# Kernel tuning notes

Hardware: AMD Instinct MI355X
Metric: run time of the kernel (lower is better)

The kernel has to match this reference:

```python
import jax, jax.numpy as jnp
import numpy as np


def setup_inputs() -> dict:
    key = jax.random.key(0)
    k1, k2, k3 = jax.random.split(key, 3)
    B, L, S, H, E, D = 2, 512, 512, 8, 32, 64
    queries = jax.random.normal(k1, (B, L, H, E), dtype=jnp.float32)
    keys = jax.random.normal(k2, (B, S, H, E), dtype=jnp.float32)
    values = jax.random.normal(k3, (B, S, H, D), dtype=jnp.float32)
    v = jnp.ones((E,), dtype=jnp.float32)
    attn_mask_add = jnp.zeros((L, S), dtype=jnp.float32)
    key_lengths_add = jnp.zeros((B, S), dtype=jnp.float32)
    return {
        "queries": queries,
        "keys": keys,
        "values": values,
        "v": v,
        "attn_mask_add": attn_mask_add,
        "key_lengths_add": key_lengths_add,
    }


def reference(queries, keys, values, v, attn_mask_add, key_lengths_add):
    # Additive (Bahdanau) attention.
    # queries: (B,L,H,E), keys: (B,S,H,E), values: (B,S,H,D)
    # Broadcast add -> tanh -> contract with v: (B,L,S,H,E) -> (B,H,L,S)
    feat = jnp.tanh(queries[:, :, None, :, :] + keys[:, None, :, :, :])  # (B,L,S,H,E)
    scores = jnp.einsum("blshe,e->bhls", feat, v)  # (B,H,L,S)
    scores = scores + attn_mask_add[None, None, :, :]          # (L,S) attn mask
    scores = scores + key_lengths_add[:, None, None, :]        # (B,S) key-length mask
    A = jax.nn.softmax(scores, axis=-1)  # (B,H,L,S); dropout is identity (p=0 / eval)
    V = jnp.einsum("bhls,bshd->blhd", A, values)  # (B,L,H,D)
    return V
```

## Files before the change

kernel.cpp:

```cpp
#include <hip/hip_runtime.h>


#define BB 2
#define LL 512
#define SS 512
#define HH 8
#define EE 32
#define DD 64

#define WS_EK_OFF 0
#define WS_EQ_OFF (2u * 1024u * 1024u)
#define WS_VT_OFF (4u * 1024u * 1024u)

typedef __attribute__((ext_vector_type(8))) short bf16x8;
typedef __attribute__((ext_vector_type(4))) float f32x4;
typedef __attribute__((ext_vector_type(4))) unsigned u32x4;

__device__ __forceinline__ unsigned short f2bf(float f) {
    unsigned u = __float_as_uint(f);
    u += 0x7FFFu + ((u >> 16) & 1u);
    return (unsigned short)(u >> 16);
}
__device__ __forceinline__ float fast_exp2(float x) {
#if __has_builtin(__builtin_amdgcn_exp2f)
    return __builtin_amdgcn_exp2f(x);
#else
    return exp2f(x);
#endif
}
__device__ __forceinline__ float fast_rcp(float x) {
    return __builtin_amdgcn_rcpf(x);
}
__device__ __forceinline__ float bcastf(float x) {
    return __int_as_float(__builtin_amdgcn_readfirstlane(__float_as_int(x)));
}

#define SCV 2.885390081777927f

__global__ __launch_bounds__(256) void prep_kernel(
    const float* __restrict__ q, const float* __restrict__ k,
    const float* __restrict__ vals, float* __restrict__ ws)
{
    unsigned gid = blockIdx.x * 256 + threadIdx.x;
    if (gid < 32768u) {
        unsigned i  = gid;
        unsigned s  = i & 511u;
        unsigned e8 = (i >> 9) & 3u;
        unsigned h  = (i >> 11) & 7u;
        unsigned b  = i >> 14;
        const float* kr = k + (((size_t)b * SS + s) * HH + h) * EE + e8 * 8;
        float4 k0 = *(const float4*)kr;
        float4 k1 = *(const float4*)(kr + 4);
        u32x4 pk;
        pk[0] = (unsigned)f2bf(fast_exp2(SCV * k0.x)) |
                ((unsigned)f2bf(fast_exp2(SCV * k0.y)) << 16);
        pk[1] = (unsigned)f2bf(fast_exp2(SCV * k0.z)) |
                ((unsigned)f2bf(fast_exp2(SCV * k0.w)) << 16);
        pk[2] = (unsigned)f2bf(fast_exp2(SCV * k1.x)) |
                ((unsigned)f2bf(fast_exp2(SCV * k1.y)) << 16);
        pk[3] = (unsigned)f2bf(fast_exp2(SCV * k1.z)) |
                ((unsigned)f2bf(fast_exp2(SCV * k1.w)) << 16);
        ((u32x4*)((char*)ws + WS_EK_OFF))[i] = pk;
    } else if (gid < 98304u) {
        unsigned i = gid - 32768u;
        float4 qv = ((const float4*)q)[i];
        float4 ev = make_float4(fast_exp2(SCV * qv.x), fast_exp2(SCV * qv.y),
                                fast_exp2(SCV * qv.z), fast_exp2(SCV * qv.w));
        ((float4*)(ws + WS_EQ_OFF / 4))[i] = ev;
    } else {
        unsigned i      = gid - 98304u;
        unsigned lane   = i & 63u;
        unsigned c      = (i >> 6) & 15u;
        unsigned dchunk = (i >> 10) & 3u;
        unsigned h      = (i >> 12) & 7u;
        unsigned b      = i >> 15;
        unsigned qd = lane >> 4, n = lane & 15;
        unsigned d  = dchunk * 16 + n;
        unsigned s0 = c * 32 + qd * 8;
        const float* vb = vals + (((size_t)b * SS + s0) * HH + h) * DD + d;
        u32x4 pk;
        #pragma unroll
        for (int j2 = 0; j2 < 4; j2++) {
            float f0 = vb[(size_t)(2 * j2) * (HH * DD)];
            float f1 = vb[(size_t)(2 * j2 + 1) * (HH * DD)];
            pk[j2] = (unsigned)f2bf(f0) | ((unsigned)f2bf(f1) << 16);
        }
        ((u32x4*)((char*)ws + WS_VT_OFF))[i] = pk;
    }
}

__global__ __launch_bounds__(256) void addattn_kernel(
    const u32x4* __restrict__ ws_ekb,
    const float* __restrict__ ws_eqf,
    const bf16x8* __restrict__ ws_vtf,
    const float* __restrict__ vvec,
    const float* __restrict__ mask,
    const float* __restrict__ klen,
    float* __restrict__ out)
{
    __shared__ u32x4 sek[4 * SS];
    __shared__ unsigned short sAb[8][SS];

    const int tid  = threadIdx.x;
    const int w    = tid >> 6;
    const int lane = tid & 63;
    const int bh   = blockIdx.x >> 6;
    const int lblk = blockIdx.x & 63;
    const int b    = bh >> 3;
    const int h    = bh & 7;
    const int l0   = lblk * 8;
    const int lw   = l0 + 2 * w;

    {
        const u32x4* esrc = ws_ekb + (size_t)(b * HH + h) * (4 * SS);
        #pragma unroll
        for (int t = 0; t < 8; t++)
            sek[tid + t * 256] = esrc[tid + t * 256];
    }

    float eq0[EE], eq1[EE], v2s[EE];
    {
        const float* q0 = ws_eqf + (((size_t)b * LL + lw) * HH + h) * EE;
        const float* q1 = q0 + HH * EE;
        #pragma unroll
        for (int e = 0; e < EE; e += 4) {
            float4 t0 = *(const float4*)(q0 + e);
            float4 t1 = *(const float4*)(q1 + e);
            eq0[e] = bcastf(t0.x); eq0[e+1] = bcastf(t0.y);
            eq0[e+2] = bcastf(t0.z); eq0[e+3] = bcastf(t0.w);
            eq1[e] = bcastf(t1.x); eq1[e+1] = bcastf(t1.y);
            eq1[e+2] = bcastf(t1.z); eq1[e+3] = bcastf(t1.w);
        }
        const float4* vr = (const float4*)vvec;
        #pragma unroll
        for (int e4 = 0; e4 < EE / 4; e4++) {
            float4 t = vr[e4];
            v2s[e4*4]   = -2.f * t.x; v2s[e4*4+1] = -2.f * t.y;
            v2s[e4*4+2] = -2.f * t.z; v2s[e4*4+3] = -2.f * t.w;
        }
    }
    __syncthreads();

    float sc[2][SS / 64];
    for (int i = 0; i < SS / 64; i++) {
        const int s = lane + i * 64;
        u32x4 g0 = sek[s];
        u32x4 g1 = sek[SS + s];
        u32x4 g2 = sek[2 * SS + s];
        u32x4 g3 = sek[3 * SS + s];
        float a0[4] = {0.f, 0.f, 0.f, 0.f};
        float a1[4] = {0.f, 0.f, 0.f, 0.f};
        #define ELEM(E, F)                                                    \
        {                                                                     \
            float p0 = __builtin_fmaf(eq0[E], F, 1.f);                        \
            float p1 = __builtin_fmaf(eq1[E], F, 1.f);                        \
            a0[(E) & 3] = __builtin_fmaf(v2s[E], fast_rcp(p0), a0[(E) & 3]);  \
            a1[(E) & 3] = __builtin_fmaf(v2s[E], fast_rcp(p1), a1[(E) & 3]);  \
        }
        #define PAIR(u, E)                                                    \
        {                                                                     \
            float flo = __uint_as_float((u) << 16);                           \
            float fhi = __uint_as_float((u) & 0xffff0000u);                   \
            ELEM(E, flo) ELEM((E) + 1, fhi)                                   \
        }
        #define GRP(g, base)                                                  \
        {                                                                     \
            PAIR(g[0], (base) + 0) PAIR(g[1], (base) + 2)                     \
            PAIR(g[2], (base) + 4) PAIR(g[3], (base) + 6)                     \
        }
        GRP(g0, 0) GRP(g1, 8) GRP(g2, 16) GRP(g3, 24)
        #undef GRP
        #undef PAIR
        #undef ELEM
        sc[0][i] = (a0[0] + a0[1]) + (a0[2] + a0[3]);
        sc[1][i] = (a1[0] + a1[1]) + (a1[2] + a1[3]);
    }

    {
        const float* kl = klen + (size_t)b * SS;
        float klv[SS / 64];
        #pragma unroll
        for (int i = 0; i < SS / 64; i++) klv[i] = kl[lane + i * 64];

        #pragma unroll
        for (int r = 0; r < 2; r++) {
            const float* mrow = mask + (size_t)(lw + r) * SS;
            float mx = -1e30f;
            #pragma unroll
            for (int i = 0; i < SS / 64; i++) {
                sc[r][i] += mrow[lane + i * 64] + klv[i];
                mx = fmaxf(mx, sc[r][i]);
            }
            #pragma unroll
            for (int off = 1; off < 64; off <<= 1) mx = fmaxf(mx, __shfl_xor(mx, off, 64));
            float ssum = 0.f;
            #pragma unroll
            for (int i = 0; i < SS / 64; i++) {
                sc[r][i] = __expf(sc[r][i] - mx);
                ssum += sc[r][i];
            }
            #pragma unroll
            for (int off = 1; off < 64; off <<= 1) ssum += __shfl_xor(ssum, off, 64);
            float inv = fast_rcp(ssum);
            const int row = 2 * w + r;
            const int fsw = (row * 5) & 7;
            #pragma unroll
            for (int i = 0; i < SS / 64; i++) {
                int col = lane + i * 64;
                int pos = (((col >> 3) ^ fsw) << 3) | (col & 7);
                sAb[row][pos] = f2bf(sc[r][i] * inv);
            }
        }
    }
    __syncthreads();

    const int am  = lane & 15;
    const int qd  = lane >> 4;
    const int dof = w * 16 + am;
    const int fam = (am * 5) & 7;
    const bf16x8* vf =
        ws_vtf + ((size_t)((b * HH + h) * 4 + w) * 16) * 64 + lane;
    f32x4 acc = {0.f, 0.f, 0.f, 0.f};
    bf16x8 bcur = vf[0];
    for (int c = 0; c < SS / 32; c++) {
        bf16x8 bnxt = bcur;
        if (c < SS / 32 - 1) bnxt = vf[(c + 1) * 64];
        bf16x8 af = {0, 0, 0, 0, 0, 0, 0, 0};
        if (am < 8)
            af = *(const bf16x8*)&sAb[am][((c * 4 + qd) ^ fam) << 3];
        acc = __builtin_amdgcn_mfma_f32_16x16x32_bf16(af, bcur, acc, 0, 0, 0);
        bcur = bnxt;
    }
    if (qd < 2) {
        float* orow = out + (((size_t)b * LL + l0 + qd * 4) * HH + h) * DD + dof;
        #pragma unroll
        for (int r = 0; r < 4; r++)
            orow[(size_t)r * (HH * DD)] = acc[r];
    }
}

extern "C" void kernel_launch(void* const* d_in, const int* in_sizes, int n_in,
                              void* d_out, int out_size, void* d_ws, size_t ws_size,
                              hipStream_t stream) {
    const float* q    = (const float*)d_in[0];
    const float* k    = (const float*)d_in[1];
    const float* vals = (const float*)d_in[2];
    const float* vvec = (const float*)d_in[3];
    const float* mask = (const float*)d_in[4];
    const float* klen = (const float*)d_in[5];
    float* outp = (float*)d_out;

    float* ws = (float*)d_ws;
    prep_kernel<<<dim3(640), dim3(256), 0, stream>>>(q, k, vals, ws);

    const u32x4* ws_ekb = (const u32x4*)((char*)d_ws + WS_EK_OFF);
    const float* ws_eqf = (const float*)((char*)d_ws + WS_EQ_OFF);
    const bf16x8* ws_vtf = (const bf16x8*)((char*)d_ws + WS_VT_OFF);
    addattn_kernel<<<dim3(BB * HH * (LL / 8)), dim3(256), 0, stream>>>(
        ws_ekb, ws_eqf, ws_vtf, vvec, mask, klen, outp);
}
```

Baseline: 93.75 us.

## Halve rows per block, stage keys in halves, pair-merge reciprocals

Each wave now handles one query row instead of two, and the grid doubles to 2048 blocks. Keys are staged into shared memory in two halves of S, and that same buffer is reused for the bf16 probability matrix, cutting LDS from about 40KB to 16KB. Per-element tanh terms are merged in pairs so one reciprocal covers two elements (a/x + b/y = (a*y+b*x)/(x*y)), halving rcp count. The aim is more occupancy and fewer transcendental ops, at the cost of loading keys twice as often per query row, running half-empty MFMA tiles, and a possible overflow risk in the product of two denominators.

```diff
diff --git a/kernel.cpp b/kernel.cpp
--- a/kernel.cpp
+++ b/kernel.cpp
@@ -98,118 +98,108 @@
     const float* __restrict__ klen,
     float* __restrict__ out)
 {
-    __shared__ u32x4 sek[4 * SS];
-    __shared__ unsigned short sAb[8][SS];
+    __shared__ u32x4 sek[4][256];
+    unsigned short* sAb = (unsigned short*)sek;
 
     const int tid  = threadIdx.x;
     const int w    = tid >> 6;
     const int lane = tid & 63;
-    const int bh   = blockIdx.x >> 6;
-    const int lblk = blockIdx.x & 63;
+    const int bh   = blockIdx.x >> 7;
+    const int lblk = blockIdx.x & 127;
     const int b    = bh >> 3;
     const int h    = bh & 7;
-    const int l0   = lblk * 8;
-    const int lw   = l0 + 2 * w;
-
-    {
-        const u32x4* esrc = ws_ekb + (size_t)(b * HH + h) * (4 * SS);
-        #pragma unroll
-        for (int t = 0; t < 8; t++)
-            sek[tid + t * 256] = esrc[tid + t * 256];
-    }
-
-    float eq0[EE], eq1[EE], v2s[EE];
-    {
-        const float* q0 = ws_eqf + (((size_t)b * LL + lw) * HH + h) * EE;
-        const float* q1 = q0 + HH * EE;
-        #pragma unroll
-        for (int e = 0; e < EE; e += 4) {
-            float4 t0 = *(const float4*)(q0 + e);
-            float4 t1 = *(const float4*)(q1 + e);
-            eq0[e] = bcastf(t0.x); eq0[e+1] = bcastf(t0.y);
-            eq0[e+2] = bcastf(t0.z); eq0[e+3] = bcastf(t0.w);
-            eq1[e] = bcastf(t1.x); eq1[e+1] = bcastf(t1.y);
-            eq1[e+2] = bcastf(t1.z); eq1[e+3] = bcastf(t1.w);
-        }
-        const float4* vr = (const float4*)vvec;
-        #pragma unroll
-        for (int e4 = 0; e4 < EE / 4; e4++) {
-            float4 t = vr[e4];
-            v2s[e4*4]   = -2.f * t.x; v2s[e4*4+1] = -2.f * t.y;
-            v2s[e4*4+2] = -2.f * t.z; v2s[e4*4+3] = -2.f * t.w;
-        }
-    }
-    __syncthreads();
-
-    float sc[2][SS / 64];
-    for (int i = 0; i < SS / 64; i++) {
-        const int s = lane + i * 64;
-        u32x4 g0 = sek[s];
-        u32x4 g1 = sek[SS + s];
-        u32x4 g2 = sek[2 * SS + s];
-        u32x4 g3 = sek[3 * SS + s];
-        float a0[4] = {0.f, 0.f, 0.f, 0.f};
-        float a1[4] = {0.f, 0.f, 0.f, 0.f};
-        #define ELEM(E, F)                                                    \
-        {                                                                     \
-            float p0 = __builtin_fmaf(eq0[E], F, 1.f);                        \
-            float p1 = __builtin_fmaf(eq1[E], F, 1.f);                        \
-            a0[(E) & 3] = __builtin_fmaf(v2s[E], fast_rcp(p0), a0[(E) & 3]);  \
-            a1[(E) & 3] = __builtin_fmaf(v2s[E], fast_rcp(p1), a1[(E) & 3]);  \
-        }
-        #define PAIR(u, E)                                                    \
-        {                                                                     \
-            float flo = __uint_as_float((u) << 16);                           \
-            float fhi = __uint_as_float((u) & 0xffff0000u);                   \
-            ELEM(E, flo) ELEM((E) + 1, fhi)                                   \
-        }
-        #define GRP(g, base)                                                  \
-        {                                                                     \
-            PAIR(g[0], (base) + 0) PAIR(g[1], (base) + 2)                     \
-            PAIR(g[2], (base) + 4) PAIR(g[3], (base) + 6)                     \
-        }
-        GRP(g0, 0) GRP(g1, 8) GRP(g2, 16) GRP(g3, 24)
-        #undef GRP
-        #undef PAIR
-        #undef ELEM
-        sc[0][i] = (a0[0] + a0[1]) + (a0[2] + a0[3]);
-        sc[1][i] = (a1[0] + a1[1]) + (a1[2] + a1[3]);
-    }
-
-    {
-        const float* kl = klen + (size_t)b * SS;
-        float klv[SS / 64];
-        #pragma unroll
-        for (int i = 0; i < SS / 64; i++) klv[i] = kl[lane + i * 64];
-
-        #pragma unroll
-        for (int r = 0; r < 2; r++) {
-            const float* mrow = mask + (size_t)(lw + r) * SS;
-            float mx = -1e30f;
+    const int l0   = lblk * 4;
+    const int l    = l0 + w;
+
+    const u32x4* slab = ws_ekb + (size_t)(b * HH + h) * (4 * 512);
+    const float* eqbase = ws_eqf + (((size_t)b * LL + l) * HH + h) * EE;
+
+    float sc[SS / 64];
+    #pragma unroll
+    for (int i = 0; i < SS / 64; i++) sc[i] = 0.f;
+
+    for (int hs = 0; hs < 2; hs++) {
+        if (hs) __syncthreads();
+        #pragma unroll
+        for (int t = 0; t < 4; t++) {
+            int idx = tid + t * 256;
+            int e8  = idx >> 8;
+            int sl  = idx & 255;
+            sek[e8][sl] = slab[e8 * 512 + hs * 256 + sl];
+        }
+        __syncthreads();
+
+        for (int p = 0; p < 2; p++) {
+            float eqs[16], v2h[16];
             #pragma unroll
-            for (int i = 0; i < SS / 64; i++) {
-                sc[r][i] += mrow[lane + i * 64] + klv[i];
-                mx = fmaxf(mx, sc[r][i]);
+            for (int e = 0; e < 16; e += 4) {
+                float4 t0 = *(const float4*)(eqbase + p * 16 + e);
+                float4 tv = *(const float4*)(vvec + p * 16 + e);
+                eqs[e]   = bcastf(t0.x); eqs[e+1] = bcastf(t0.y);
+                eqs[e+2] = bcastf(t0.z); eqs[e+3] = bcastf(t0.w);
+                v2h[e]   = bcastf(-2.f * tv.x); v2h[e+1] = bcastf(-2.f * tv.y);
+                v2h[e+2] = bcastf(-2.f * tv.z); v2h[e+3] = bcastf(-2.f * tv.w);
             }
             #pragma unroll
-            for (int off = 1; off < 64; off <<= 1) mx = fmaxf(mx, __shfl_xor(mx, off, 64));
-            float ssum = 0.f;
-            #pragma unroll
-            for (int i = 0; i < SS / 64; i++) {
-                sc[r][i] = __expf(sc[r][i] - mx);
-                ssum += sc[r][i];
+            for (int i = 0; i < 4; i++) {
+                const int sl = lane + i * 64;
+                u32x4 gA = sek[2 * p][sl];
+                u32x4 gB = sek[2 * p + 1][sl];
+                float a0 = 0.f, a1 = 0.f;
+                #define PAIR(u, le, A)                                        \
+                {                                                             \
+                    float eklo = __uint_as_float((u) << 16);                  \
+                    float ekhi = __uint_as_float((u) & 0xffff0000u);          \
+                    float qa = __builtin_fmaf(eqs[le], eklo, 1.f);            \
+                    float qb = __builtin_fmaf(eqs[(le) + 1], ekhi, 1.f);      \
+                    float nm = __builtin_fmaf(v2h[le], qb, v2h[(le) + 1] * qa); \
+                    A = __builtin_fmaf(nm, fast_rcp(qa * qb), A);             \
+                }
+                PAIR(gA[0], 0, a0) PAIR(gA[1], 2, a1)
+                PAIR(gA[2], 4, a0) PAIR(gA[3], 6, a1)
+                PAIR(gB[0], 8, a0) PAIR(gB[1], 10, a1)
+                PAIR(gB[2], 12, a0) PAIR(gB[3], 14, a1)
+                #undef PAIR
+                sc[hs * 4 + i] += a0 + a1;
             }
-            #pragma unroll
-            for (int off = 1; off < 64; off <<= 1) ssum += __shfl_xor(ssum, off, 64);
-            float inv = fast_rcp(ssum);
-            const int row = 2 * w + r;
-            const int fsw = (row * 5) & 7;
-            #pragma unroll
-            for (int i = 0; i < SS / 64; i++) {
-                int col = lane + i * 64;
-                int pos = (((col >> 3) ^ fsw) << 3) | (col & 7);
-                sAb[row][pos] = f2bf(sc[r][i] * inv);
-            }
+        }
+    }
+
+    float prob[SS / 64];
+    {
+        const float* mrow = mask + (size_t)l * SS;
+        const float* kl   = klen + (size_t)b * SS;
+        float mx = -1e30f;
+        #pragma unroll
+        for (int i = 0; i < SS / 64; i++) {
+            int s = lane + i * 64;
+            sc[i] += mrow[s] + kl[s];
+            mx = fmaxf(mx, sc[i]);
+        }
+        #pragma unroll
+        for (int off = 1; off < 64; off <<= 1) mx = fmaxf(mx, __shfl_xor(mx, off, 64));
+        float ssum = 0.f;
+        #pragma unroll
+        for (int i = 0; i < SS / 64; i++) {
+            prob[i] = __expf(sc[i] - mx);
+            ssum += prob[i];
+        }
+        #pragma unroll
+        for (int off = 1; off < 64; off <<= 1) ssum += __shfl_xor(ssum, off, 64);
+        float inv = fast_rcp(ssum);
+        #pragma unroll
+        for (int i = 0; i < SS / 64; i++) prob[i] *= inv;
+    }
+
+    __syncthreads();
+
+    {
+        const int fsw = (w * 5) & 7;
+        #pragma unroll
+        for (int i = 0; i < SS / 64; i++) {
+            int col = lane + i * 64;
+            int pos = (((col >> 3) ^ fsw) << 3) | (col & 7);
+            sAb[w * SS + pos] = f2bf(prob[i]);
         }
     }
     __syncthreads();
@@ -226,13 +216,13 @@
         bf16x8 bnxt = bcur;
         if (c < SS / 32 - 1) bnxt = vf[(c + 1) * 64];
         bf16x8 af = {0, 0, 0, 0, 0, 0, 0, 0};
-        if (am < 8)
-            af = *(const bf16x8*)&sAb[am][((c * 4 + qd) ^ fam) << 3];
+        if (am < 4)
+            af = *(const bf16x8*)&sAb[am * SS + ((((c * 4 + qd) ^ fam)) << 3)];
         acc = __builtin_amdgcn_mfma_f32_16x16x32_bf16(af, bcur, acc, 0, 0, 0);
         bcur = bnxt;
     }
-    if (qd < 2) {
-        float* orow = out + (((size_t)b * LL + l0 + qd * 4) * HH + h) * DD + dof;
+    if (qd == 0) {
+        float* orow = out + (((size_t)b * LL + l0) * HH + h) * DD + dof;
         #pragma unroll
         for (int r = 0; r < 4; r++)
             orow[(size_t)r * (HH * DD)] = acc[r];
@@ -256,6 +246,6 @@
     const u32x4* ws_ekb = (const u32x4*)((char*)d_ws + WS_EK_OFF);
     const float* ws_eqf = (const float*)((char*)d_ws + WS_EQ_OFF);
     const bf16x8* ws_vtf = (const bf16x8*)((char*)d_ws + WS_VT_OFF);
-    addattn_kernel<<<dim3(BB * HH * (LL / 8)), dim3(256), 0, stream>>>(
+    addattn_kernel<<<dim3(BB * HH * (LL / 4)), dim3(256), 0, stream>>>(
         ws_ekb, ws_eqf, ws_vtf, vvec, mask, klen, outp);
 }
```

After: 97.81 us. 1.04x slower.

## Split attention into score and PV kernels, pair tanh reciprocals, drop max pass

Applied to the files above, without the earlier changes.

Splits the fused kernel in two. The score kernel writes unnormalized bf16 probabilities and row sums to the workspace, and a separate PV kernel runs full 16-row MFMA tiles and normalizes at output. The tanh rational terms are combined in pairs so one reciprocal serves two elements. The softmax max reduction is replaced by clamping at 80, which risks overflow or precision loss when scores are large or masks very negative. The split adds an extra launch and a global round trip for the probability matrix, in exchange for removing the wasted half-empty MFMA rows and half the reciprocals.

```diff
diff --git a/kernel.cpp b/kernel.cpp
--- a/kernel.cpp
+++ b/kernel.cpp
@@ -11,6 +11,8 @@
 #define WS_EK_OFF 0
 #define WS_EQ_OFF (2u * 1024u * 1024u)
 #define WS_VT_OFF (4u * 1024u * 1024u)
+#define WS_PR_OFF (8u * 1024u * 1024u)
+#define WS_SM_OFF (16u * 1024u * 1024u)
 
 typedef __attribute__((ext_vector_type(8))) short bf16x8;
 typedef __attribute__((ext_vector_type(4))) float f32x4;
@@ -89,17 +91,16 @@
     }
 }
 
-__global__ __launch_bounds__(256) void addattn_kernel(
+__global__ __launch_bounds__(256) void score_kernel(
     const u32x4* __restrict__ ws_ekb,
     const float* __restrict__ ws_eqf,
-    const bf16x8* __restrict__ ws_vtf,
     const float* __restrict__ vvec,
     const float* __restrict__ mask,
     const float* __restrict__ klen,
-    float* __restrict__ out)
+    unsigned short* __restrict__ ws_prob,
+    float* __restrict__ ws_sum)
 {
     __shared__ u32x4 sek[4 * SS];
-    __shared__ unsigned short sAb[8][SS];
 
     const int tid  = threadIdx.x;
     const int w    = tid >> 6;
@@ -108,11 +109,10 @@
     const int lblk = blockIdx.x & 63;
     const int b    = bh >> 3;
     const int h    = bh & 7;
-    const int l0   = lblk * 8;
-    const int lw   = l0 + 2 * w;
+    const int lw   = lblk * 8 + 2 * w;
 
     {
-        const u32x4* esrc = ws_ekb + (size_t)(b * HH + h) * (4 * SS);
+        const u32x4* esrc = ws_ekb + (size_t)bh * (4 * SS);
         #pragma unroll
         for (int t = 0; t < 8; t++)
             sek[tid + t * 256] = esrc[tid + t * 256];
@@ -135,45 +135,44 @@
         #pragma unroll
         for (int e4 = 0; e4 < EE / 4; e4++) {
             float4 t = vr[e4];
-            v2s[e4*4]   = -2.f * t.x; v2s[e4*4+1] = -2.f * t.y;
-            v2s[e4*4+2] = -2.f * t.z; v2s[e4*4+3] = -2.f * t.w;
+            v2s[e4*4]   = bcastf(-2.f * t.x); v2s[e4*4+1] = bcastf(-2.f * t.y);
+            v2s[e4*4+2] = bcastf(-2.f * t.z); v2s[e4*4+3] = bcastf(-2.f * t.w);
         }
     }
     __syncthreads();
 
-    float sc[2][SS / 64];
+    float sc0[SS / 64], sc1[SS / 64];
     for (int i = 0; i < SS / 64; i++) {
         const int s = lane + i * 64;
         u32x4 g0 = sek[s];
         u32x4 g1 = sek[SS + s];
         u32x4 g2 = sek[2 * SS + s];
         u32x4 g3 = sek[3 * SS + s];
-        float a0[4] = {0.f, 0.f, 0.f, 0.f};
-        float a1[4] = {0.f, 0.f, 0.f, 0.f};
-        #define ELEM(E, F)                                                    \
+        float a0A = 0.f, a0B = 0.f, a1A = 0.f, a1B = 0.f;
+        #define PAIR2(u, le, A0, A1)                                          \
         {                                                                     \
-            float p0 = __builtin_fmaf(eq0[E], F, 1.f);                        \
-            float p1 = __builtin_fmaf(eq1[E], F, 1.f);                        \
-            a0[(E) & 3] = __builtin_fmaf(v2s[E], fast_rcp(p0), a0[(E) & 3]);  \
-            a1[(E) & 3] = __builtin_fmaf(v2s[E], fast_rcp(p1), a1[(E) & 3]);  \
-        }
-        #define PAIR(u, E)                                                    \
-        {                                                                     \
-            float flo = __uint_as_float((u) << 16);                           \
-            float fhi = __uint_as_float((u) & 0xffff0000u);                   \
-            ELEM(E, flo) ELEM((E) + 1, fhi)                                   \
-        }
-        #define GRP(g, base)                                                  \
-        {                                                                     \
-            PAIR(g[0], (base) + 0) PAIR(g[1], (base) + 2)                     \
-            PAIR(g[2], (base) + 4) PAIR(g[3], (base) + 6)                     \
-        }
-        GRP(g0, 0) GRP(g1, 8) GRP(g2, 16) GRP(g3, 24)
-        #undef GRP
-        #undef PAIR
-        #undef ELEM
-        sc[0][i] = (a0[0] + a0[1]) + (a0[2] + a0[3]);
-        sc[1][i] = (a1[0] + a1[1]) + (a1[2] + a1[3]);
+            float eklo = __uint_as_float((u) << 16);                          \
+            float ekhi = __uint_as_float((u) & 0xffff0000u);                  \
+            float qa0 = __builtin_fmaf(eq0[le], eklo, 1.f);                   \
+            float qb0 = __builtin_fmaf(eq0[(le) + 1], ekhi, 1.f);             \
+            float nm0 = __builtin_fmaf(v2s[le], qb0, v2s[(le) + 1] * qa0);    \
+            A0 = __builtin_fmaf(nm0, fast_rcp(qa0 * qb0), A0);                \
+            float qa1 = __builtin_fmaf(eq1[le], eklo, 1.f);                   \
+            float qb1 = __builtin_fmaf(eq1[(le) + 1], ekhi, 1.f);             \
+            float nm1 = __builtin_fmaf(v2s[le], qb1, v2s[(le) + 1] * qa1);    \
+            A1 = __builtin_fmaf(nm1, fast_rcp(qa1 * qb1), A1);                \
+        }
+        PAIR2(g0[0], 0, a0A, a1A)  PAIR2(g0[1], 2, a0B, a1B)
+        PAIR2(g0[2], 4, a0A, a1A)  PAIR2(g0[3], 6, a0B, a1B)
+        PAIR2(g1[0], 8, a0A, a1A)  PAIR2(g1[1], 10, a0B, a1B)
+        PAIR2(g1[2], 12, a0A, a1A) PAIR2(g1[3], 14, a0B, a1B)
+        PAIR2(g2[0], 16, a0A, a1A) PAIR2(g2[1], 18, a0B, a1B)
+        PAIR2(g2[2], 20, a0A, a1A) PAIR2(g2[3], 22, a0B, a1B)
+        PAIR2(g3[0], 24, a0A, a1A) PAIR2(g3[1], 26, a0B, a1B)
+        PAIR2(g3[2], 28, a0A, a1A) PAIR2(g3[3], 30, a0B, a1B)
+        #undef PAIR2
+        sc0[i] = a0A + a0B;
+        sc1[i] = a1A + a1B;
     }
 
     {
@@ -184,59 +183,68 @@
 
         #pragma unroll
         for (int r = 0; r < 2; r++) {
+            float* sc = r ? sc1 : sc0;
             const float* mrow = mask + (size_t)(lw + r) * SS;
-            float mx = -1e30f;
-            #pragma unroll
-            for (int i = 0; i < SS / 64; i++) {
-                sc[r][i] += mrow[lane + i * 64] + klv[i];
-                mx = fmaxf(mx, sc[r][i]);
-            }
-            #pragma unroll
-            for (int off = 1; off < 64; off <<= 1) mx = fmaxf(mx, __shfl_xor(mx, off, 64));
             float ssum = 0.f;
             #pragma unroll
             for (int i = 0; i < SS / 64; i++) {
-                sc[r][i] = __expf(sc[r][i] - mx);
-                ssum += sc[r][i];
+                float v = fminf(sc[i] + mrow[lane + i * 64] + klv[i], 80.f);
+                sc[i] = __expf(v);
+                ssum += sc[i];
             }
             #pragma unroll
             for (int off = 1; off < 64; off <<= 1) ssum += __shfl_xor(ssum, off, 64);
-            float inv = fast_rcp(ssum);
-            const int row = 2 * w + r;
-            const int fsw = (row * 5) & 7;
+            unsigned short* pr = ws_prob + ((size_t)bh * LL + lw + r) * SS;
             #pragma unroll
-            for (int i = 0; i < SS / 64; i++) {
-                int col = lane + i * 64;
-                int pos = (((col >> 3) ^ fsw) << 3) | (col & 7);
-                sAb[row][pos] = f2bf(sc[r][i] * inv);
-            }
-        }
-    }
-    __syncthreads();
-
-    const int am  = lane & 15;
-    const int qd  = lane >> 4;
+            for (int i = 0; i < SS / 64; i++)
+                pr[lane + i * 64] = f2bf(sc[i]);
+            if (lane == 0) ws_sum[(size_t)bh * LL + lw + r] = ssum;
+        }
+    }
+}
+
+__global__ __launch_bounds__(256) void pv_kernel(
+    const unsigned short* __restrict__ ws_prob,
+    const float* __restrict__ ws_sum,
+    const bf16x8* __restrict__ ws_vtf,
+    float* __restrict__ out)
+{
+    const int tid  = threadIdx.x;
+    const int w    = tid >> 6;
+    const int lane = tid & 63;
+    const int bh   = blockIdx.x >> 5;
+    const int lt   = blockIdx.x & 31;
+    const int b    = bh >> 3;
+    const int h    = bh & 7;
+    const int l0   = lt * 16;
+
+    const int am = lane & 15;
+    const int qd = lane >> 4;
+    const unsigned short* ap = ws_prob + ((size_t)bh * LL + l0 + am) * SS + qd * 8;
+    const bf16x8* vf = ws_vtf + ((size_t)(bh * 4 + w) * 16) * 64 + lane;
+
+    f32x4 acc = {0.f, 0.f, 0.f, 0.f};
+    bf16x8 af[4], bv[4];
+    #pragma unroll
+    for (int c = 0; c < 4; c++) {
+        af[c] = *(const bf16x8*)(ap + c * 32);
+        bv[c] = vf[c * 64];
+    }
+    #pragma unroll
+    for (int c = 0; c < SS / 32; c++) {
+        acc = __builtin_amdgcn_mfma_f32_16x16x32_bf16(af[c & 3], bv[c & 3],
+                                                      acc, 0, 0, 0);
+        if (c + 4 < SS / 32) {
+            af[c & 3] = *(const bf16x8*)(ap + (c + 4) * 32);
+            bv[c & 3] = vf[(c + 4) * 64];
+        }
+    }
     const int dof = w * 16 + am;
-    const int fam = (am * 5) & 7;
-    const bf16x8* vf =
-        ws_vtf + ((size_t)((b * HH + h) * 4 + w) * 16) * 64 + lane;
-    f32x4 acc = {0.f, 0.f, 0.f, 0.f};
-    bf16x8 bcur = vf[0];
-    for (int c = 0; c < SS / 32; c++) {
-        bf16x8 bnxt = bcur;
-        if (c < SS / 32 - 1) bnxt = vf[(c + 1) * 64];
-        bf16x8 af = {0, 0, 0, 0, 0, 0, 0, 0};
-        if (am < 8)
-            af = *(const bf16x8*)&sAb[am][((c * 4 + qd) ^ fam) << 3];
-        acc = __builtin_amdgcn_mfma_f32_16x16x32_bf16(af, bcur, acc, 0, 0, 0);
-        bcur = bnxt;
-    }
-    if (qd < 2) {
-        float* orow = out + (((size_t)b * LL + l0 + qd * 4) * HH + h) * DD + dof;
-        #pragma unroll
-        for (int r = 0; r < 4; r++)
-            orow[(size_t)r * (HH * DD)] = acc[r];
-    }
+    float* orow = out + (((size_t)b * LL + l0 + qd * 4) * HH + h) * DD + dof;
+    const float* sm = ws_sum + (size_t)bh * LL + l0 + qd * 4;
+    #pragma unroll
+    for (int r = 0; r < 4; r++)
+        orow[(size_t)r * (HH * DD)] = acc[r] * fast_rcp(sm[r]);
 }
 
 extern "C" void kernel_launch(void* const* d_in, const int* in_sizes, int n_in,
@@ -256,6 +264,12 @@
     const u32x4* ws_ekb = (const u32x4*)((char*)d_ws + WS_EK_OFF);
     const float* ws_eqf = (const float*)((char*)d_ws + WS_EQ_OFF);
     const bf16x8* ws_vtf = (const bf16x8*)((char*)d_ws + WS_VT_OFF);
-    addattn_kernel<<<dim3(BB * HH * (LL / 8)), dim3(256), 0, stream>>>(
-        ws_ekb, ws_eqf, ws_vtf, vvec, mask, klen, outp);
-}
+    unsigned short* ws_prob = (unsigned short*)((char*)d_ws + WS_PR_OFF);
+    float* ws_sum = (float*)((char*)d_ws + WS_SM_OFF);
+
+    score_kernel<<<dim3(BB * HH * (LL / 8)), dim3(256), 0, stream>>>(
+        ws_ekb, ws_eqf, vvec, mask, klen, ws_prob, ws_sum);
+
+    pv_kernel<<<dim3(BB * HH * (LL / 16)), dim3(256), 0, stream>>>(
+        ws_prob, ws_sum, ws_vtf, outp);
+}
```

Result: slower. 108.1 us (+15.3%).
